# Performance work log

Hardware: AMD Instinct MI355X
Metric: run time of the kernel (lower is better)

## Reference

```python
import jax, jax.numpy as jnp
import numpy as np

DN = ('NCDHW', 'DHWIO', 'NCDHW')
EPS = 1e-5


def conv_s2(x, W):
    # ME kernel-3 stride-2 conv: out[o] = sum_{d in {-1,0,1}^3} W[d] @ in[2o+d]
    return jax.lax.conv_general_dilated(x, W, (2, 2, 2), ((1, 1),) * 3,
                                        dimension_numbers=DN)


def deconv_s2(x, W):
    # ME kernel-3 stride-2 transpose conv: out[2i+d] += W[d] @ in[i]
    # == zero-stuffed (lhs_dilation=2) conv with spatially flipped kernel.
    Wf = W[::-1, ::-1, ::-1]
    return jax.lax.conv_general_dilated(x, Wf, (1, 1, 1), ((1, 2),) * 3,
                                        lhs_dilation=(2, 2, 2),
                                        dimension_numbers=DN)


def pool2(m):
    # output coordinate existence for stride-2: any occupied voxel in 2x2x2 block
    return jax.lax.reduce_window(m, 0.0, jax.lax.max,
                                 (1, 1, 2, 2, 2), (1, 1, 2, 2, 2), 'VALID')


def bn_relu(x, m, gamma, beta):
    # MinkowskiBatchNorm: stats over occupied points only (mask m in {0,1})
    cnt = m.sum()
    mean = (x * m).sum(axis=(0, 2, 3, 4)) / cnt            # [C]
    xc = (x - mean[None, :, None, None, None]) * m
    var = (xc * xc).sum(axis=(0, 2, 3, 4)) / cnt           # biased var, [C]
    scale = (gamma / jnp.sqrt(var + EPS))[None, :, None, None, None]
    y = xc * scale + beta[None, :, None, None, None] * m
    return jax.nn.relu(y) * m


def occ_head(x, m, w, b):
    # 1x1 conv (C->1, bias) + sigmoid at occupied sites
    logit = jnp.einsum('bcdhw,c->bdhw', x, w)[:, None] + b
    return jax.nn.sigmoid(logit) * m


def setup_inputs() -> dict:
    key = jax.random.key(0)
    ks = jax.random.split(key, 24)
    B, Cin, Cout, G = 2, 3, 3, 96
    feats = jax.random.normal(ks[0], (B, Cin, G, G, G), jnp.float32)
    mask = jax.random.bernoulli(ks[1], 0.2, (B, 1, G, G, G))

    def w(k, ci, co):
        return jax.random.normal(k, (3, 3, 3, ci, co), jnp.float32) * np.float32((2.0 / (27 * co)) ** 0.5)

    enc = [16, 32, 64, 128]
    d = {'feats': feats, 'mask': mask}
    d['W1'] = w(ks[2], Cin, 16); d['g1'] = jnp.ones(16); d['b1'] = jnp.zeros(16)
    d['W2'] = w(ks[3], 16, 32);  d['g2'] = jnp.ones(32); d['b2'] = jnp.zeros(32)
    d['W3'] = w(ks[4], 32, 64);  d['g3'] = jnp.ones(64); d['b3'] = jnp.zeros(64)
    d['W4'] = w(ks[5], 64, 128); d['g4'] = jnp.ones(128); d['b4'] = jnp.zeros(128)
    d['Wt4'] = w(ks[6], 128, 64); d['gd4'] = jnp.ones(64); d['bd4'] = jnp.zeros(64)
    d['wo4'] = jax.random.normal(ks[7], (64,), jnp.float32) * 0.1; d['bo4'] = jnp.zeros((1,))
    d['Wt3'] = w(ks[8], 64, 32); d['gd3'] = jnp.ones(32); d['bd3'] = jnp.zeros(32)
    d['wo3'] = jax.random.normal(ks[9], (32,), jnp.float32) * 0.1; d['bo3'] = jnp.zeros((1,))
    d['Wt2'] = w(ks[10], 32, 16); d['gd2'] = jnp.ones(16); d['bd2'] = jnp.zeros(16)
    d['wo2'] = jax.random.normal(ks[11], (16,), jnp.float32) * 0.1; d['bo2'] = jnp.zeros((1,))
    d['Wt1'] = w(ks[12], 16, Cout)
    d['wo1'] = jax.random.normal(ks[13], (Cout,), jnp.float32) * 0.1; d['bo1'] = jnp.zeros((1,))
    return d


def reference(feats, mask, W1, g1, b1, W2, g2, b2, W3, g3, b3, W4, g4, b4,
              Wt4, gd4, bd4, wo4, bo4, Wt3, gd3, bd3, wo3, bo3,
              Wt2, gd2, bd2, wo2, bo2, Wt1, wo1, bo1):
    m0 = mask.astype(feats.dtype)
    m1 = pool2(m0); m2 = pool2(m1); m3 = pool2(m2); m4 = pool2(m3)
    x = feats * m0
    e0 = bn_relu(conv_s2(x, W1), m1, g1, b1)    # [B,16,48^3]
    e1 = bn_relu(conv_s2(e0, W2), m2, g2, b2)   # [B,32,24^3]
    e2 = bn_relu(conv_s2(e1, W3), m3, g3, b3)   # [B,64,12^3]
    e3 = bn_relu(conv_s2(e2, W4), m4, g4, b4)   # [B,128,6^3]
    d3 = bn_relu(deconv_s2(e3, Wt4), m3, gd4, bd4)
    p4 = occ_head(d3, m3, wo4, bo4)
    d3 = d3 + e2
    d2 = bn_relu(deconv_s2(d3, Wt3), m2, gd3, bd3)
    p3 = occ_head(d2, m2, wo3, bo3)
    d2 = d2 + e1
    d1 = bn_relu(deconv_s2(d2, Wt2), m1, gd2, bd2)
    p2 = occ_head(d1, m1, wo2, bo2)
    d1 = d1 + e0
    d0 = jax.nn.sigmoid(deconv_s2(d1, Wt1)) * m0  # Decoder1: transpose conv + sigmoid
    p1 = occ_head(d0, m0, wo1, bo1)
    return (d0, p4, p3, p2, p1)
```

## Files before the change

kernel.cpp:

```cpp
#include <hip/hip_runtime.h>
#include <math.h>

#define CDIV(a,b) (((a)+(b)-1)/(b))
typedef unsigned int u32;

__device__ __forceinline__ float sigmoidf_(float x) { return 1.f / (1.f + __expf(-x)); }

__global__ void k_detect(const u32* __restrict__ w, int n, u32* __restrict__ flag) {
    u32 local = 0;
    for (int i = blockIdx.x * blockDim.x + threadIdx.x; i < n; i += gridDim.x * blockDim.x) {
        u32 v = w[i];
        if (v == 0x3F800000u) local |= 2u;
        else if (v > 1u)      local |= 1u;
    }
    if (local) atomicOr(flag, local);
}

__global__ void k_expand(const void* __restrict__ mraw, const u32* __restrict__ flag,
                         float* __restrict__ m, int n) {
    int i = blockIdx.x * blockDim.x + threadIdx.x;
    if (i >= n) return;
    u32 f = *flag;
    float v;
    if (f & 2u)      v = ((const float*)mraw)[i];
    else if (f & 1u) v = ((const unsigned char*)mraw)[i] ? 1.f : 0.f;
    else             v = ((const int*)mraw)[i] ? 1.f : 0.f;
    m[i] = v;
}

__global__ void k_pool(const float* __restrict__ mi, float* __restrict__ mo,
                       float* __restrict__ cnt, int Si, int n) {
    int So = Si >> 1;
    int i = blockIdx.x * blockDim.x + threadIdx.x;
    float v = 0.f;
    if (i < n) {
        int x = i % So; int t = i / So;
        int y = t % So; t /= So;
        int z = t % So; int b = t / So;
        const float* p = mi + (size_t)b * Si * Si * Si;
        #pragma unroll
        for (int dz = 0; dz < 2; dz++)
        #pragma unroll
        for (int dy = 0; dy < 2; dy++)
        #pragma unroll
        for (int dx = 0; dx < 2; dx++) {
            float q = p[((size_t)(2 * z + dz) * Si + (2 * y + dy)) * Si + (2 * x + dx)];
            v = fmaxf(v, q);
        }
        mo[i] = v;
    }
    __shared__ float red[256];
    red[threadIdx.x] = v; __syncthreads();
    for (int s = 128; s > 0; s >>= 1) {
        if (threadIdx.x < s) red[threadIdx.x] += red[threadIdx.x + s];
        __syncthreads();
    }
    if (threadIdx.x == 0) atomicAdd(cnt, red[0]);
}

__global__ __launch_bounds__(256)
void k_conv1(const float* __restrict__ feats, const float* __restrict__ m0,
             const float* __restrict__ W, float* __restrict__ out,
             const float* __restrict__ m1, float* __restrict__ stats) {
    constexpr int SIN = 96;
    constexpr int V0 = SIN * SIN * SIN, V1 = 48 * 48 * 48;
    __shared__ __align__(16) float wlds[27 * 3 * 16];
    __shared__ float sred[4][32];
    for (int idx = threadIdx.x; idx < 27 * 3 * 16; idx += 256) wlds[idx] = W[idx];
    __syncthreads();
    int chunk = blockIdx.x * 256 + threadIdx.x;
    int b = chunk / V1; int s = chunk - b * V1;
    int x = s % 48, y = (s / 48) % 48, z = s / 2304;
    float acc[16];
    #pragma unroll
    for (int co = 0; co < 16; ++co) acc[co] = 0.f;
    const float* bi = feats + (size_t)b * 3 * V0;
    const float* bm = m0 + (size_t)b * V0;
    #pragma unroll
    for (int kz = 0; kz < 3; ++kz) {
        int iz = 2 * z - 1 + kz; if (iz < 0) continue;
        #pragma unroll
        for (int ky = 0; ky < 3; ++ky) {
            int iy = 2 * y - 1 + ky; if (iy < 0) continue;
            #pragma unroll
            for (int kx = 0; kx < 3; ++kx) {
                int ix = 2 * x - 1 + kx; if (ix < 0) continue;
                int off = (iz * SIN + iy) * SIN + ix;
                float mv = bm[off];
                if (mv != 0.f) {
                    float f0 = bi[off], f1 = bi[V0 + off], f2 = bi[2 * V0 + off];
                    const float* wp = &wlds[((kz * 3 + ky) * 3 + kx) * 48];
                    #pragma unroll
                    for (int co = 0; co < 16; ++co)
                        acc[co] += f0 * wp[co] + f1 * wp[16 + co] + f2 * wp[32 + co];
                }
            }
        }
    }
    float mm = m1[chunk];
    #pragma unroll
    for (int co = 0; co < 16; ++co) acc[co] *= mm;
    float* op = out + (size_t)chunk * 16;
    #pragma unroll
    for (int q = 0; q < 4; ++q)
        *reinterpret_cast<float4*>(op + q * 4) =
            make_float4(acc[q*4], acc[q*4+1], acc[q*4+2], acc[q*4+3]);
    float s1[16], s2[16];
    #pragma unroll
    for (int co = 0; co < 16; ++co) { s1[co] = acc[co]; s2[co] = acc[co] * acc[co]; }
    #pragma unroll
    for (int co = 0; co < 16; ++co)
        for (int off = 1; off < 64; off <<= 1) {
            s1[co] += __shfl_xor(s1[co], off);
            s2[co] += __shfl_xor(s2[co], off);
        }
    int lane = threadIdx.x & 63, wid = threadIdx.x >> 6;
    if (lane == 0) {
        #pragma unroll
        for (int co = 0; co < 16; ++co) { sred[wid][co] = s1[co]; sred[wid][16 + co] = s2[co]; }
    }
    __syncthreads();
    if (threadIdx.x < 32) {
        int t = threadIdx.x;
        float v = sred[0][t] + sred[1][t] + sred[2][t] + sred[3][t];
        int addr = (t < 16) ? t : (128 + t - 16);
        atomicAdd(&stats[addr], v);
    }
}

template<int CI, int CO, int CO_T, int SIN, int SOUT, bool STATS>
__global__ __launch_bounds__(256)
void k_convCL(const float* __restrict__ in, const float* __restrict__ W,
              float* __restrict__ out, const float* __restrict__ mout,
              float* __restrict__ stats) {
    constexpr int SIN3 = SIN * SIN * SIN, SOUT3 = SOUT * SOUT * SOUT;
    constexpr int NW = 27 * CI * CO_T;
    __shared__ __align__(16) float wlds[NW];
    __shared__ float sred[STATS ? 4 : 1][2 * CO_T];
    const int cobase = blockIdx.y * CO_T;
    for (int idx = threadIdx.x; idx < NW; idx += 256) {
        int t = idx / (CI * CO_T);
        int rem = idx - t * CI * CO_T;
        int ci = rem / CO_T, co = rem - ci * CO_T;
        wlds[idx] = W[(size_t)(t * CI + ci) * CO + cobase + co];
    }
    __syncthreads();
    int chunk = blockIdx.x * 256 + threadIdx.x;
    bool active = chunk < 2 * SOUT3;
    if (!STATS && !active) return;
    float acc[CO_T];
    #pragma unroll
    for (int co = 0; co < CO_T; ++co) acc[co] = 0.f;
    if (active) {
        int b = chunk / SOUT3, s = chunk - b * SOUT3;
        int x = s % SOUT, y = (s / SOUT) % SOUT, z = s / (SOUT * SOUT);
        const float* bi = in + (size_t)b * SIN3 * CI;
        #pragma unroll
        for (int kz = 0; kz < 3; ++kz) {
            int iz = 2 * z - 1 + kz; if (iz < 0 || iz >= SIN) continue;
            #pragma unroll
            for (int ky = 0; ky < 3; ++ky) {
                int iy = 2 * y - 1 + ky; if (iy < 0 || iy >= SIN) continue;
                #pragma unroll
                for (int kx = 0; kx < 3; ++kx) {
                    int ix = 2 * x - 1 + kx; if (ix < 0 || ix >= SIN) continue;
                    const float* p = bi + (size_t)((iz * SIN + iy) * SIN + ix) * CI;
                    const float* wp = &wlds[((kz * 3 + ky) * 3 + kx) * CI * CO_T];
                    #pragma unroll
                    for (int cq = 0; cq < CI / 4; ++cq) {
                        float4 v = *reinterpret_cast<const float4*>(p + cq * 4);
                        const float* wq = wp + cq * 4 * CO_T;
                        float vv[4] = {v.x, v.y, v.z, v.w};
                        #pragma unroll
                        for (int jj = 0; jj < 4; ++jj)
                        #pragma unroll
                        for (int co = 0; co < CO_T; ++co)
                            acc[co] += vv[jj] * wq[jj * CO_T + co];
                    }
                }
            }
        }
        float mm = mout[chunk];
        #pragma unroll
        for (int co = 0; co < CO_T; ++co) acc[co] *= mm;
        float* op = out + (size_t)chunk * CO + cobase;
        #pragma unroll
        for (int q = 0; q < CO_T / 4; ++q)
            *reinterpret_cast<float4*>(op + q * 4) =
                make_float4(acc[q*4], acc[q*4+1], acc[q*4+2], acc[q*4+3]);
    }
    if constexpr (STATS) {
        float s1[CO_T], s2[CO_T];
        #pragma unroll
        for (int co = 0; co < CO_T; ++co) { s1[co] = acc[co]; s2[co] = acc[co] * acc[co]; }
        #pragma unroll
        for (int co = 0; co < CO_T; ++co)
            for (int off = 1; off < 64; off <<= 1) {
                s1[co] += __shfl_xor(s1[co], off);
                s2[co] += __shfl_xor(s2[co], off);
            }
        int lane = threadIdx.x & 63, wid = threadIdx.x >> 6;
        if (lane == 0) {
            #pragma unroll
            for (int co = 0; co < CO_T; ++co) { sred[wid][co] = s1[co]; sred[wid][CO_T + co] = s2[co]; }
        }
        __syncthreads();
        if (threadIdx.x < 2 * CO_T) {
            int t = threadIdx.x;
            float v = sred[0][t] + sred[1][t] + sred[2][t] + sred[3][t];
            int addr = (t < CO_T) ? (cobase + t) : (128 + cobase + t - CO_T);
            atomicAdd(&stats[addr], v);
        }
    }
}

template<int CI, int CO, int CO_T, int SIN, bool STATS>
__global__ __launch_bounds__(256)
void k_deconvG(const float* __restrict__ in, const float* __restrict__ W,
               const float* __restrict__ mout, float* __restrict__ out,
               float* __restrict__ stats) {
    constexpr int SOUT = 2 * SIN;
    constexpr int SIN3 = SIN * SIN * SIN, SOUT3 = SOUT * SOUT * SOUT;
    constexpr int NW = 27 * CI * CO_T;
    __shared__ __align__(16) float wlds[NW];
    __shared__ float sred[STATS ? 4 : 1][2 * CO_T];
    const int cobase = blockIdx.y * CO_T;
    for (int idx = threadIdx.x; idx < NW; idx += 256) {
        int w = idx / (CI * CO_T);
        int rem = idx - w * (CI * CO_T);
        int ci = rem / CO_T, co = rem - ci * CO_T;
        wlds[idx] = W[(size_t)(w * CI + ci) * CO + cobase + co];
    }
    __syncthreads();
    int chunk = blockIdx.x * 256 + threadIdx.x;
    bool active = chunk < 2 * SOUT3;
    if (!STATS && !active) return;
    float acc[CO_T];
    #pragma unroll
    for (int co = 0; co < CO_T; ++co) acc[co] = 0.f;
    if (active) {
        int b = chunk / SOUT3, s = chunk - b * SOUT3;
        int x = s % SOUT, y = (s / SOUT) % SOUT, z = s / (SOUT * SOUT);
        int z0 = z >> 1, y0 = y >> 1, x0 = x >> 1;
        int nz = ((z & 1) && (z0 + 1 < SIN)) ? 2 : 1;
        int ny = ((y & 1) && (y0 + 1 < SIN)) ? 2 : 1;
        int nx = ((x & 1) && (x0 + 1 < SIN)) ? 2 : 1;
        int wz0 = (z & 1) ? 2 : 1, wy0 = (y & 1) ? 2 : 1, wx0 = (x & 1) ? 2 : 1;
        const float* bi = in + (size_t)b * SIN3 * CI;
        #pragma unroll 1
        for (int tz = 0; tz < nz; ++tz) {
            int iz = z0 + tz, wz = tz ? 0 : wz0;
            #pragma unroll 1
            for (int ty = 0; ty < ny; ++ty) {
                int iy = y0 + ty, wy = ty ? 0 : wy0;
                #pragma unroll 1
                for (int tx = 0; tx < nx; ++tx) {
                    int ix = x0 + tx, wx = tx ? 0 : wx0;
                    const float* p = bi + (size_t)((iz * SIN + iy) * SIN + ix) * CI;
                    const float* wb = &wlds[((wz * 3 + wy) * 3 + wx) * CI * CO_T];
                    #pragma unroll 8
                    for (int cq = 0; cq < CI / 4; ++cq) {
                        float4 v = *reinterpret_cast<const float4*>(p + cq * 4);
                        const float* wq = wb + cq * 4 * CO_T;
                        float vv[4] = {v.x, v.y, v.z, v.w};
                        #pragma unroll
                        for (int jj = 0; jj < 4; ++jj)
                        #pragma unroll
                        for (int co = 0; co < CO_T; ++co)
                            acc[co] += vv[jj] * wq[jj * CO_T + co];
                    }
                }
            }
        }
        float mm = mout[chunk];
        #pragma unroll
        for (int co = 0; co < CO_T; ++co) acc[co] *= mm;
        float* op = out + (size_t)chunk * CO + cobase;
        #pragma unroll
        for (int q = 0; q < CO_T / 4; ++q)
            *reinterpret_cast<float4*>(op + q * 4) =
                make_float4(acc[q*4], acc[q*4+1], acc[q*4+2], acc[q*4+3]);
    }
    if constexpr (STATS) {
        float s1[CO_T], s2[CO_T];
        #pragma unroll
        for (int co = 0; co < CO_T; ++co) { s1[co] = acc[co]; s2[co] = acc[co] * acc[co]; }
        #pragma unroll
        for (int co = 0; co < CO_T; ++co)
            for (int off = 1; off < 64; off <<= 1) {
                s1[co] += __shfl_xor(s1[co], off);
                s2[co] += __shfl_xor(s2[co], off);
            }
        int lane = threadIdx.x & 63, wid = threadIdx.x >> 6;
        if (lane == 0) {
            #pragma unroll
            for (int co = 0; co < CO_T; ++co) { sred[wid][co] = s1[co]; sred[wid][CO_T + co] = s2[co]; }
        }
        __syncthreads();
        if (threadIdx.x < 2 * CO_T) {
            int t = threadIdx.x;
            float v = sred[0][t] + sred[1][t] + sred[2][t] + sred[3][t];
            int addr = (t < CO_T) ? (cobase + t) : (128 + cobase + t - CO_T);
            atomicAdd(&stats[addr], v);
        }
    }
}

__global__ __launch_bounds__(256)
void k_deconv_final(const float* __restrict__ in, const float* __restrict__ W,
                    const float* __restrict__ m0, float* __restrict__ out,
                    const float* __restrict__ ow, const float* __restrict__ ob,
                    float* __restrict__ p1out) {
    constexpr int SI = 48, SO = 96;
    constexpr int SI3 = SI * SI * SI, SO3 = SO * SO * SO;
    __shared__ __align__(16) float wlds[27 * 16 * 4];
    for (int idx = threadIdx.x; idx < 27 * 16 * 4; idx += 256) {
        int w = idx >> 6; int rem = idx & 63;
        int ci = rem >> 2, co = rem & 3;
        wlds[idx] = (co < 3) ? W[(size_t)(w * 16 + ci) * 3 + co] : 0.f;
    }
    __syncthreads();
    int t = blockIdx.x * 256 + threadIdx.x;
    int b = t / (SO3 / 4); int s = t - b * (SO3 / 4);
    int x4 = s % 24; int y = (s / 24) % SO; int z = s / (24 * SO);
    int x0 = x4 * 4, kxb = x4 * 2;
    int izs[2], wzs[2], nz = 1;
    if (z & 1) { izs[0] = z >> 1; wzs[0] = 2; int i2 = (z >> 1) + 1;
                 if (i2 < SI) { izs[1] = i2; wzs[1] = 0; nz = 2; } }
    else       { izs[0] = z >> 1; wzs[0] = 1; }
    int iys[2], wys[2], ny = 1;
    if (y & 1) { iys[0] = y >> 1; wys[0] = 2; int i2 = (y >> 1) + 1;
                 if (i2 < SI) { iys[1] = i2; wys[1] = 0; ny = 2; } }
    else       { iys[0] = y >> 1; wys[0] = 1; }
    bool has2 = (kxb + 2 < SI);
    float acc[4][3];
    #pragma unroll
    for (int o = 0; o < 4; ++o)
    #pragma unroll
    for (int c = 0; c < 3; ++c) acc[o][c] = 0.f;
    const float* bi = in + (size_t)b * SI3 * 16;
    #pragma unroll 1
    for (int tz = 0; tz < nz; ++tz)
    #pragma unroll 1
    for (int ty = 0; ty < ny; ++ty) {
        const float* vp = bi + ((size_t)(izs[tz] * SI + iys[ty]) * SI + kxb) * 16;
        float v[3][16];
        #pragma unroll
        for (int q = 0; q < 4; ++q) {
            float4 a = *reinterpret_cast<const float4*>(vp + q * 4);
            float4 bq = *reinterpret_cast<const float4*>(vp + 16 + q * 4);
            v[0][q*4] = a.x; v[0][q*4+1] = a.y; v[0][q*4+2] = a.z; v[0][q*4+3] = a.w;
            v[1][q*4] = bq.x; v[1][q*4+1] = bq.y; v[1][q*4+2] = bq.z; v[1][q*4+3] = bq.w;
            float4 cq = has2 ? *reinterpret_cast<const float4*>(vp + 32 + q * 4)
                             : make_float4(0.f, 0.f, 0.f, 0.f);
            v[2][q*4] = cq.x; v[2][q*4+1] = cq.y; v[2][q*4+2] = cq.z; v[2][q*4+3] = cq.w;
        }
        const float* wb = &wlds[(wzs[tz] * 3 + wys[ty]) * 3 * 64];
        #pragma unroll
        for (int ci = 0; ci < 16; ++ci) {
            float4 w0 = *reinterpret_cast<const float4*>(wb + ci * 4);
            float4 w1 = *reinterpret_cast<const float4*>(wb + 64 + ci * 4);
            float4 w2 = *reinterpret_cast<const float4*>(wb + 128 + ci * 4);
            float v0 = v[0][ci], v1 = v[1][ci], v2 = v[2][ci];
            acc[0][0] += v0 * w1.x; acc[0][1] += v0 * w1.y; acc[0][2] += v0 * w1.z;
            acc[1][0] += v0 * w2.x + v1 * w0.x;
            acc[1][1] += v0 * w2.y + v1 * w0.y;
            acc[1][2] += v0 * w2.z + v1 * w0.z;
            acc[2][0] += v1 * w1.x; acc[2][1] += v1 * w1.y; acc[2][2] += v1 * w1.z;
            acc[3][0] += v1 * w2.x + v2 * w0.x;
            acc[3][1] += v1 * w2.y + v2 * w0.y;
            acc[3][2] += v1 * w2.z + v2 * w0.z;
        }
    }
    int row = (z * SO + y) * SO + x0;
    float4 mm = *reinterpret_cast<const float4*>(m0 + (size_t)b * SO3 + row);
    float mv[4] = {mm.x, mm.y, mm.z, mm.w};
    const float w0o = ow[0], w1o = ow[1], w2o = ow[2], bo = ob[0];
    float yv[3][4], p1[4];
    #pragma unroll
    for (int o = 0; o < 4; ++o) {
        float y0 = sigmoidf_(acc[o][0]) * mv[o];
        float y1 = sigmoidf_(acc[o][1]) * mv[o];
        float y2 = sigmoidf_(acc[o][2]) * mv[o];
        yv[0][o] = y0; yv[1][o] = y1; yv[2][o] = y2;
        p1[o] = sigmoidf_(y0 * w0o + y1 * w1o + y2 * w2o + bo) * mv[o];
    }
    float* ob0 = out + (size_t)b * 3 * SO3 + row;
    #pragma unroll
    for (int c = 0; c < 3; ++c)
        *reinterpret_cast<float4*>(ob0 + (size_t)c * SO3) =
            make_float4(yv[c][0], yv[c][1], yv[c][2], yv[c][3]);
    *reinterpret_cast<float4*>(p1out + (size_t)b * SO3 + row) =
        make_float4(p1[0], p1[1], p1[2], p1[3]);
}

template<int C, bool OCC, bool ADD>
__global__ __launch_bounds__(256)
void k_bnCL(float* __restrict__ x, const float* __restrict__ m,
            const float* __restrict__ stats, const float* __restrict__ cnt,
            const float* __restrict__ g, const float* __restrict__ be,
            const float* __restrict__ skip, const float* __restrict__ ow,
            const float* __restrict__ ob, float* __restrict__ oo, int totq) {
    constexpr int CQ = C / 4;
    int i = blockIdx.x * 256 + threadIdx.x;
    if (i >= totq) return;
    int vox = i / CQ, cq = i - vox * CQ;
    int c0 = 4 * cq;
    float cn = *cnt;
    float4 s1 = *reinterpret_cast<const float4*>(stats + c0);
    float4 s2 = *reinterpret_cast<const float4*>(stats + 128 + c0);
    float sc[4], sh[4];
    {
        float mean0 = s1.x / cn, mean1 = s1.y / cn, mean2 = s1.z / cn, mean3 = s1.w / cn;
        float v0 = s2.x / cn - mean0 * mean0, v1 = s2.y / cn - mean1 * mean1;
        float v2 = s2.z / cn - mean2 * mean2, v3 = s2.w / cn - mean3 * mean3;
        sc[0] = g[c0] * rsqrtf(v0 + 1e-5f);   sh[0] = be[c0] - mean0 * sc[0];
        sc[1] = g[c0+1] * rsqrtf(v1 + 1e-5f); sh[1] = be[c0+1] - mean1 * sc[1];
        sc[2] = g[c0+2] * rsqrtf(v2 + 1e-5f); sh[2] = be[c0+2] - mean2 * sc[2];
        sc[3] = g[c0+3] * rsqrtf(v3 + 1e-5f); sh[3] = be[c0+3] - mean3 * sc[3];
    }
    float mm = m[vox];
    float4 xv = *reinterpret_cast<const float4*>(x + (size_t)i * 4);
    float y[4];
    y[0] = fmaxf(xv.x * sc[0] + sh[0], 0.f) * mm;
    y[1] = fmaxf(xv.y * sc[1] + sh[1], 0.f) * mm;
    y[2] = fmaxf(xv.z * sc[2] + sh[2], 0.f) * mm;
    y[3] = fmaxf(xv.w * sc[3] + sh[3], 0.f) * mm;
    if constexpr (OCC) {
        float po = y[0] * ow[c0] + y[1] * ow[c0+1] + y[2] * ow[c0+2] + y[3] * ow[c0+3];
        #pragma unroll
        for (int off = 1; off < CQ; off <<= 1) po += __shfl_xor(po, off);
        if (cq == 0) oo[vox] = sigmoidf_(po + ob[0]) * mm;
    }
    if constexpr (ADD) {
        float4 sk = *reinterpret_cast<const float4*>(skip + (size_t)i * 4);
        y[0] += sk.x; y[1] += sk.y; y[2] += sk.z; y[3] += sk.w;
    }
    *reinterpret_cast<float4*>(x + (size_t)i * 4) = make_float4(y[0], y[1], y[2], y[3]);
}

extern "C" void kernel_launch(void* const* d_in, const int* in_sizes, int n_in,
                              void* d_out, int out_size, void* d_ws, size_t ws_size,
                              hipStream_t stream) {
    (void)in_sizes; (void)n_in; (void)out_size; (void)ws_size;
    const float* feats = (const float*)d_in[0];
    const void*  mraw  = d_in[1];
    const float* W1 = (const float*)d_in[2];
    const float* g1 = (const float*)d_in[3];  const float* b1 = (const float*)d_in[4];
    const float* W2 = (const float*)d_in[5];
    const float* g2 = (const float*)d_in[6];  const float* b2 = (const float*)d_in[7];
    const float* W3 = (const float*)d_in[8];
    const float* g3 = (const float*)d_in[9];  const float* b3 = (const float*)d_in[10];
    const float* W4 = (const float*)d_in[11];
    const float* g4 = (const float*)d_in[12]; const float* b4 = (const float*)d_in[13];
    const float* Wt4 = (const float*)d_in[14];
    const float* gd4 = (const float*)d_in[15]; const float* bd4 = (const float*)d_in[16];
    const float* wo4 = (const float*)d_in[17]; const float* bo4 = (const float*)d_in[18];
    const float* Wt3 = (const float*)d_in[19];
    const float* gd3 = (const float*)d_in[20]; const float* bd3 = (const float*)d_in[21];
    const float* wo3 = (const float*)d_in[22]; const float* bo3 = (const float*)d_in[23];
    const float* Wt2 = (const float*)d_in[24];
    const float* gd2 = (const float*)d_in[25]; const float* bd2 = (const float*)d_in[26];
    const float* wo2 = (const float*)d_in[27]; const float* bo2 = (const float*)d_in[28];
    const float* Wt1 = (const float*)d_in[29];
    const float* wo1 = (const float*)d_in[30]; const float* bo1 = (const float*)d_in[31];

    float* out = (float*)d_out;

    const int NB = 2;
    const int V0 = 96 * 96 * 96;
    const int V1 = 48 * 48 * 48;
    const int V2 = 24 * 24 * 24;
    const int V3 = 12 * 12 * 12;
    const int V4 = 6 * 6 * 6;

    const size_t OFF_P4 = (size_t)NB * 3 * V0;
    const size_t OFF_P3 = OFF_P4 + (size_t)NB * V3;
    const size_t OFF_P2 = OFF_P3 + (size_t)NB * V2;
    const size_t OFF_P1 = OFF_P2 + (size_t)NB * V1;

    float* ws = (float*)d_ws;
    size_t o = 0;
    auto alloc = [&](size_t n) { float* p = ws + o; o += ((n + 63) / 64) * 64; return p; };
    u32*   flag  = (u32*)alloc(64);
    float* cnt   = alloc(64);
    float* stats = alloc(8 * 512);
    float* m0f   = alloc((size_t)NB * V0);
    float* m1f   = alloc((size_t)NB * V1);
    float* m2f   = alloc((size_t)NB * V2);
    float* m3f   = alloc((size_t)NB * V3);
    float* m4f   = alloc((size_t)NB * V4);
    float* e0    = alloc((size_t)NB * V1 * 16);
    float* e1    = alloc((size_t)NB * V2 * 32);
    float* e2    = alloc((size_t)NB * V3 * 64);
    float* e3    = alloc((size_t)NB * V4 * 128);
    float* d3    = alloc((size_t)NB * V3 * 64);
    float* d2    = alloc((size_t)NB * V2 * 32);
    float* d1    = alloc((size_t)NB * V1 * 16);
    (void)alloc(1024);

    const int T = 256;

    hipMemsetAsync(flag, 0, (64 + 64 + 8 * 512) * sizeof(float), stream);

    k_detect<<<256, T, 0, stream>>>((const u32*)mraw, (NB * V0) / 4, flag);
    k_expand<<<CDIV(NB * V0, T), T, 0, stream>>>(mraw, flag, m0f, NB * V0);
    k_pool<<<CDIV(NB * V1, T), T, 0, stream>>>(m0f, m1f, &cnt[0], 96, NB * V1);
    k_pool<<<CDIV(NB * V2, T), T, 0, stream>>>(m1f, m2f, &cnt[1], 48, NB * V2);
    k_pool<<<CDIV(NB * V3, T), T, 0, stream>>>(m2f, m3f, &cnt[2], 24, NB * V3);
    k_pool<<<CDIV(NB * V4, T), T, 0, stream>>>(m3f, m4f, &cnt[3], 12, NB * V4);

    k_conv1<<<864, T, 0, stream>>>(feats, m0f, W1, e0, m1f, stats + 0 * 512);
    k_bnCL<16, false, false><<<3456, T, 0, stream>>>(
        e0, m1f, stats + 0 * 512, &cnt[0], g1, b1, nullptr, nullptr, nullptr, nullptr, NB * V1 * 4);

    k_convCL<16, 32, 8, 48, 24, true><<<dim3(108, 4), T, 0, stream>>>(
        e0, W2, e1, m2f, stats + 1 * 512);
    k_bnCL<32, false, false><<<864, T, 0, stream>>>(
        e1, m2f, stats + 1 * 512, &cnt[1], g2, b2, nullptr, nullptr, nullptr, nullptr, NB * V2 * 8);

    k_convCL<32, 64, 4, 24, 12, true><<<dim3(14, 16), T, 0, stream>>>(
        e1, W3, e2, m3f, stats + 2 * 512);
    k_bnCL<64, false, false><<<216, T, 0, stream>>>(
        e2, m3f, stats + 2 * 512, &cnt[2], g3, b3, nullptr, nullptr, nullptr, nullptr, NB * V3 * 16);

    k_convCL<64, 128, 4, 12, 6, true><<<dim3(2, 32), T, 0, stream>>>(
        e2, W4, e3, m4f, stats + 3 * 512);
    k_bnCL<128, false, false><<<54, T, 0, stream>>>(
        e3, m4f, stats + 3 * 512, &cnt[3], g4, b4, nullptr, nullptr, nullptr, nullptr, NB * V4 * 32);

    k_deconvG<128, 64, 4, 6, true><<<dim3(14, 16), T, 0, stream>>>(
        e3, Wt4, m3f, d3, stats + 4 * 512);
    k_bnCL<64, true, true><<<216, T, 0, stream>>>(
        d3, m3f, stats + 4 * 512, &cnt[2], gd4, bd4, e2, wo4, bo4, out + OFF_P4, NB * V3 * 16);

    k_deconvG<64, 32, 8, 12, true><<<dim3(108, 4), T, 0, stream>>>(
        d3, Wt3, m2f, d2, stats + 5 * 512);
    k_bnCL<32, true, true><<<864, T, 0, stream>>>(
        d2, m2f, stats + 5 * 512, &cnt[1], gd3, bd3, e1, wo3, bo3, out + OFF_P3, NB * V2 * 8);

    k_deconvG<32, 16, 16, 24, true><<<dim3(864, 1), T, 0, stream>>>(
        d2, Wt2, m1f, d1, stats + 6 * 512);
    k_bnCL<16, true, true><<<3456, T, 0, stream>>>(
        d1, m1f, stats + 6 * 512, &cnt[0], gd2, bd2, e0, wo2, bo2, out + OFF_P2, NB * V1 * 4);

    k_deconv_final<<<1728, T, 0, stream>>>(d1, Wt1, m0f, out, wo1, bo1, out + OFF_P1);
}
```

Before: 415.8 us.

## Register-block multiple x outputs per thread in stride-2 conv and deconv kernels

Result: slower. 638.6 us (+53.6%).

```diff
diff --git a/kernel.cpp b/kernel.cpp
--- a/kernel.cpp
+++ b/kernel.cpp
@@ -125,6 +125,259 @@
         float v = sred[0][t] + sred[1][t] + sred[2][t] + sred[3][t];
         int addr = (t < 16) ? t : (128 + t - 16);
         atomicAdd(&stats[addr], v);
+    }
+}
+
+template<int CI, int CO, int CO_T, int SP_T, int SIN, int SOUT, bool STATS>
+__global__ __launch_bounds__(256)
+void k_convS(const float* __restrict__ in, const float* __restrict__ W,
+             float* __restrict__ out, const float* __restrict__ mout,
+             float* __restrict__ stats) {
+    constexpr int SIN3 = SIN * SIN * SIN, SOUT3 = SOUT * SOUT * SOUT;
+    constexpr int XG = SOUT / SP_T;
+    constexpr int NTH = 2 * SOUT * SOUT * XG;
+    constexpr int WST = CI * CO_T + 4;
+    __shared__ __align__(16) float wlds[27 * WST];
+    __shared__ float sred[4][2 * CO_T];
+    const int cobase = blockIdx.y * CO_T;
+    for (int idx = threadIdx.x; idx < 27 * CI * CO_T; idx += 256) {
+        int t = idx / (CI * CO_T);
+        int rem = idx - t * (CI * CO_T);
+        int ci = rem / CO_T, co = rem - ci * CO_T;
+        wlds[t * WST + ci * CO_T + co] = W[(size_t)(t * CI + ci) * CO + cobase + co];
+    }
+    __syncthreads();
+    int chunk = blockIdx.x * 256 + threadIdx.x;
+    bool active = chunk < NTH;
+    float acc[SP_T][CO_T];
+    #pragma unroll
+    for (int j = 0; j < SP_T; ++j)
+    #pragma unroll
+    for (int co = 0; co < CO_T; ++co) acc[j][co] = 0.f;
+    if (active) {
+        int xg = chunk % XG; int q = chunk / XG;
+        int y = q % SOUT; q /= SOUT;
+        int z = q % SOUT; int b = q / SOUT;
+        int x0 = SP_T * xg;
+        int xbi = 2 * x0 - 1;
+        const float* bi = in + (size_t)b * SIN3 * CI;
+        #pragma unroll
+        for (int kz = 0; kz < 3; ++kz) {
+            int iz = 2 * z - 1 + kz; if (iz < 0) continue;
+            #pragma unroll
+            for (int ky = 0; ky < 3; ++ky) {
+                int iy = 2 * y - 1 + ky; if (iy < 0) continue;
+                const float* rp = bi + (size_t)((iz * SIN + iy) * SIN) * CI;
+                #pragma unroll
+                for (int cq = 0; cq < CI / 4; ++cq) {
+                    float v[2 * SP_T + 1][4];
+                    #pragma unroll
+                    for (int t = 0; t < 2 * SP_T + 1; ++t) {
+                        int ix = xbi + t;
+                        float4 q4 = make_float4(0.f, 0.f, 0.f, 0.f);
+                        if (ix >= 0)
+                            q4 = *reinterpret_cast<const float4*>(rp + (size_t)ix * CI + cq * 4);
+                        v[t][0] = q4.x; v[t][1] = q4.y; v[t][2] = q4.z; v[t][3] = q4.w;
+                    }
+                    #pragma unroll
+                    for (int kx = 0; kx < 3; ++kx) {
+                        const float* wb = &wlds[((kz * 3 + ky) * 3 + kx) * WST + cq * 4 * CO_T];
+                        #pragma unroll
+                        for (int jj = 0; jj < 4; ++jj) {
+                            float wv[CO_T];
+                            #pragma unroll
+                            for (int co = 0; co < CO_T; ++co) wv[co] = wb[jj * CO_T + co];
+                            #pragma unroll
+                            for (int j = 0; j < SP_T; ++j) {
+                                float iv = v[2 * j + kx][jj];
+                                #pragma unroll
+                                for (int co = 0; co < CO_T; ++co) acc[j][co] += iv * wv[co];
+                            }
+                        }
+                    }
+                }
+            }
+        }
+        int vbase = b * SOUT3 + (z * SOUT + y) * SOUT + x0;
+        #pragma unroll
+        for (int j = 0; j < SP_T; ++j) {
+            float mm = mout[vbase + j];
+            #pragma unroll
+            for (int co = 0; co < CO_T; ++co) acc[j][co] *= mm;
+            float* op = out + (size_t)(vbase + j) * CO + cobase;
+            #pragma unroll
+            for (int q4 = 0; q4 < CO_T / 4; ++q4)
+                *reinterpret_cast<float4*>(op + q4 * 4) =
+                    make_float4(acc[j][q4*4], acc[j][q4*4+1], acc[j][q4*4+2], acc[j][q4*4+3]);
+        }
+    }
+    if constexpr (STATS) {
+        float s1[CO_T], s2[CO_T];
+        #pragma unroll
+        for (int co = 0; co < CO_T; ++co) {
+            float a = 0.f, b2 = 0.f;
+            #pragma unroll
+            for (int j = 0; j < SP_T; ++j) { a += acc[j][co]; b2 += acc[j][co] * acc[j][co]; }
+            s1[co] = a; s2[co] = b2;
+        }
+        #pragma unroll
+        for (int co = 0; co < CO_T; ++co)
+            for (int off = 1; off < 64; off <<= 1) {
+                s1[co] += __shfl_xor(s1[co], off);
+                s2[co] += __shfl_xor(s2[co], off);
+            }
+        int lane = threadIdx.x & 63, wid = threadIdx.x >> 6;
+        if (lane == 0) {
+            #pragma unroll
+            for (int co = 0; co < CO_T; ++co) { sred[wid][co] = s1[co]; sred[wid][CO_T + co] = s2[co]; }
+        }
+        __syncthreads();
+        if (threadIdx.x < 2 * CO_T) {
+            int t = threadIdx.x;
+            float v = sred[0][t] + sred[1][t] + sred[2][t] + sred[3][t];
+            int addr = (t < CO_T) ? (cobase + t) : (128 + cobase + t - CO_T);
+            atomicAdd(&stats[addr], v);
+        }
+    }
+}
+
+template<int CI, int CO, int CO_T, int SP_T, int SIN, bool STATS>
+__global__ __launch_bounds__(256)
+void k_deconvP(const float* __restrict__ in, const float* __restrict__ W,
+               const float* __restrict__ mout, float* __restrict__ out,
+               float* __restrict__ stats) {
+    constexpr int SOUT = 2 * SIN;
+    constexpr int SIN3 = SIN * SIN * SIN, SOUT3 = SOUT * SOUT * SOUT;
+    constexpr int GX = SOUT / (2 * SP_T);
+    constexpr int NTH = 2 * SOUT * SOUT * 2 * GX;
+    constexpr int HALF = NTH / 2;
+    constexpr int WST = CI * CO_T + 4;
+    __shared__ __align__(16) float wlds[27 * WST];
+    __shared__ float sred[4][2 * CO_T];
+    const int cobase = blockIdx.y * CO_T;
+    for (int idx = threadIdx.x; idx < 27 * CI * CO_T; idx += 256) {
+        int w = idx / (CI * CO_T);
+        int rem = idx - w * (CI * CO_T);
+        int ci = rem / CO_T, co = rem - ci * CO_T;
+        wlds[w * WST + ci * CO_T + co] = W[(size_t)(w * CI + ci) * CO + cobase + co];
+    }
+    __syncthreads();
+    int chunk = blockIdx.x * 256 + threadIdx.x;
+    bool active = chunk < NTH;
+    float acc[SP_T][CO_T];
+    #pragma unroll
+    for (int j = 0; j < SP_T; ++j)
+    #pragma unroll
+    for (int co = 0; co < CO_T; ++co) acc[j][co] = 0.f;
+    if (active) {
+        int p = (chunk >= HALF) ? 1 : 0;
+        int r = chunk - p * HALF;
+        int g = r % GX; int q = r / GX;
+        int y = q % SOUT; q /= SOUT;
+        int z = q % SOUT; int b = q / SOUT;
+        int xb = SP_T * g;
+        int z0 = z >> 1, y0 = y >> 1;
+        int nz = ((z & 1) && (z0 + 1 < SIN)) ? 2 : 1;
+        int ny = ((y & 1) && (y0 + 1 < SIN)) ? 2 : 1;
+        int wz0 = (z & 1) ? 2 : 1, wy0 = (y & 1) ? 2 : 1;
+        bool lastok = (xb + SP_T < SIN);
+        const float* bi = in + (size_t)b * SIN3 * CI;
+        #pragma unroll 1
+        for (int tz = 0; tz < nz; ++tz) {
+            int iz = z0 + tz, wz = tz ? 0 : wz0;
+            #pragma unroll 1
+            for (int ty = 0; ty < ny; ++ty) {
+                int iy = y0 + ty, wy = ty ? 0 : wy0;
+                const float* rp = bi + (size_t)((iz * SIN + iy) * SIN + xb) * CI;
+                #pragma unroll
+                for (int cq = 0; cq < CI / 4; ++cq) {
+                    float v[SP_T + 1][4];
+                    #pragma unroll
+                    for (int t = 0; t < SP_T; ++t) {
+                        float4 q4 = *reinterpret_cast<const float4*>(rp + (size_t)t * CI + cq * 4);
+                        v[t][0] = q4.x; v[t][1] = q4.y; v[t][2] = q4.z; v[t][3] = q4.w;
+                    }
+                    if (p) {
+                        float4 q4 = make_float4(0.f, 0.f, 0.f, 0.f);
+                        if (lastok)
+                            q4 = *reinterpret_cast<const float4*>(rp + (size_t)SP_T * CI + cq * 4);
+                        v[SP_T][0] = q4.x; v[SP_T][1] = q4.y; v[SP_T][2] = q4.z; v[SP_T][3] = q4.w;
+                    }
+                    if (p == 0) {
+                        const float* wb = &wlds[((wz * 3 + wy) * 3 + 1) * WST + cq * 4 * CO_T];
+                        #pragma unroll
+                        for (int jj = 0; jj < 4; ++jj) {
+                            float wv[CO_T];
+                            #pragma unroll
+                            for (int co = 0; co < CO_T; ++co) wv[co] = wb[jj * CO_T + co];
+                            #pragma unroll
+                            for (int j = 0; j < SP_T; ++j) {
+                                float iv = v[j][jj];
+                                #pragma unroll
+                                for (int co = 0; co < CO_T; ++co) acc[j][co] += iv * wv[co];
+                            }
+                        }
+                    } else {
+                        const float* wb2 = &wlds[((wz * 3 + wy) * 3 + 2) * WST + cq * 4 * CO_T];
+                        const float* wb0 = &wlds[((wz * 3 + wy) * 3 + 0) * WST + cq * 4 * CO_T];
+                        #pragma unroll
+                        for (int jj = 0; jj < 4; ++jj) {
+                            float wv2[CO_T], wv0[CO_T];
+                            #pragma unroll
+                            for (int co = 0; co < CO_T; ++co) { wv2[co] = wb2[jj * CO_T + co]; wv0[co] = wb0[jj * CO_T + co]; }
+                            #pragma unroll
+                            for (int j = 0; j < SP_T; ++j) {
+                                float ivA = v[j][jj], ivB = v[j + 1][jj];
+                                #pragma unroll
+                                for (int co = 0; co < CO_T; ++co)
+                                    acc[j][co] += ivA * wv2[co] + ivB * wv0[co];
+                            }
+                        }
+                    }
+                }
+            }
+        }
+        int sp = b * SOUT3 + (z * SOUT + y) * SOUT;
+        #pragma unroll
+        for (int j = 0; j < SP_T; ++j) {
+            int vox = sp + 2 * (xb + j) + p;
+            float mm = mout[vox];
+            #pragma unroll
+            for (int co = 0; co < CO_T; ++co) acc[j][co] *= mm;
+            float* op = out + (size_t)vox * CO + cobase;
+            #pragma unroll
+            for (int q4 = 0; q4 < CO_T / 4; ++q4)
+                *reinterpret_cast<float4*>(op + q4 * 4) =
+                    make_float4(acc[j][q4*4], acc[j][q4*4+1], acc[j][q4*4+2], acc[j][q4*4+3]);
+        }
+    }
+    if constexpr (STATS) {
+        float s1[CO_T], s2[CO_T];
+        #pragma unroll
+        for (int co = 0; co < CO_T; ++co) {
+            float a = 0.f, b2 = 0.f;
+            #pragma unroll
+            for (int j = 0; j < SP_T; ++j) { a += acc[j][co]; b2 += acc[j][co] * acc[j][co]; }
+            s1[co] = a; s2[co] = b2;
+        }
+        #pragma unroll
+        for (int co = 0; co < CO_T; ++co)
+            for (int off = 1; off < 64; off <<= 1) {
+                s1[co] += __shfl_xor(s1[co], off);
+                s2[co] += __shfl_xor(s2[co], off);
+            }
+        int lane = threadIdx.x & 63, wid = threadIdx.x >> 6;
+        if (lane == 0) {
+            #pragma unroll
+            for (int co = 0; co < CO_T; ++co) { sred[wid][co] = s1[co]; sred[wid][CO_T + co] = s2[co]; }
+        }
+        __syncthreads();
+        if (threadIdx.x < 2 * CO_T) {
+            int t = threadIdx.x;
+            float v = sred[0][t] + sred[1][t] + sred[2][t] + sred[3][t];
+            int addr = (t < CO_T) ? (cobase + t) : (128 + cobase + t - CO_T);
+            atomicAdd(&stats[addr], v);
+        }
     }
 }
 
@@ -170,98 +423,6 @@
                     for (int cq = 0; cq < CI / 4; ++cq) {
                         float4 v = *reinterpret_cast<const float4*>(p + cq * 4);
                         const float* wq = wp + cq * 4 * CO_T;
-                        float vv[4] = {v.x, v.y, v.z, v.w};
-                        #pragma unroll
-                        for (int jj = 0; jj < 4; ++jj)
-                        #pragma unroll
-                        for (int co = 0; co < CO_T; ++co)
-                            acc[co] += vv[jj] * wq[jj * CO_T + co];
-                    }
-                }
-            }
-        }
-        float mm = mout[chunk];
-        #pragma unroll
-        for (int co = 0; co < CO_T; ++co) acc[co] *= mm;
-        float* op = out + (size_t)chunk * CO + cobase;
-        #pragma unroll
-        for (int q = 0; q < CO_T / 4; ++q)
-            *reinterpret_cast<float4*>(op + q * 4) =
-                make_float4(acc[q*4], acc[q*4+1], acc[q*4+2], acc[q*4+3]);
-    }
-    if constexpr (STATS) {
-        float s1[CO_T], s2[CO_T];
-        #pragma unroll
-        for (int co = 0; co < CO_T; ++co) { s1[co] = acc[co]; s2[co] = acc[co] * acc[co]; }
-        #pragma unroll
-        for (int co = 0; co < CO_T; ++co)
-            for (int off = 1; off < 64; off <<= 1) {
-                s1[co] += __shfl_xor(s1[co], off);
-                s2[co] += __shfl_xor(s2[co], off);
-            }
-        int lane = threadIdx.x & 63, wid = threadIdx.x >> 6;
-        if (lane == 0) {
-            #pragma unroll
-            for (int co = 0; co < CO_T; ++co) { sred[wid][co] = s1[co]; sred[wid][CO_T + co] = s2[co]; }
-        }
-        __syncthreads();
-        if (threadIdx.x < 2 * CO_T) {
-            int t = threadIdx.x;
-            float v = sred[0][t] + sred[1][t] + sred[2][t] + sred[3][t];
-            int addr = (t < CO_T) ? (cobase + t) : (128 + cobase + t - CO_T);
-            atomicAdd(&stats[addr], v);
-        }
-    }
-}
-
-template<int CI, int CO, int CO_T, int SIN, bool STATS>
-__global__ __launch_bounds__(256)
-void k_deconvG(const float* __restrict__ in, const float* __restrict__ W,
-               const float* __restrict__ mout, float* __restrict__ out,
-               float* __restrict__ stats) {
-    constexpr int SOUT = 2 * SIN;
-    constexpr int SIN3 = SIN * SIN * SIN, SOUT3 = SOUT * SOUT * SOUT;
-    constexpr int NW = 27 * CI * CO_T;
-    __shared__ __align__(16) float wlds[NW];
-    __shared__ float sred[STATS ? 4 : 1][2 * CO_T];
-    const int cobase = blockIdx.y * CO_T;
-    for (int idx = threadIdx.x; idx < NW; idx += 256) {
-        int w = idx / (CI * CO_T);
-        int rem = idx - w * (CI * CO_T);
-        int ci = rem / CO_T, co = rem - ci * CO_T;
-        wlds[idx] = W[(size_t)(w * CI + ci) * CO + cobase + co];
-    }
-    __syncthreads();
-    int chunk = blockIdx.x * 256 + threadIdx.x;
-    bool active = chunk < 2 * SOUT3;
-    if (!STATS && !active) return;
-    float acc[CO_T];
-    #pragma unroll
-    for (int co = 0; co < CO_T; ++co) acc[co] = 0.f;
-    if (active) {
-        int b = chunk / SOUT3, s = chunk - b * SOUT3;
-        int x = s % SOUT, y = (s / SOUT) % SOUT, z = s / (SOUT * SOUT);
-        int z0 = z >> 1, y0 = y >> 1, x0 = x >> 1;
-        int nz = ((z & 1) && (z0 + 1 < SIN)) ? 2 : 1;
-        int ny = ((y & 1) && (y0 + 1 < SIN)) ? 2 : 1;
-        int nx = ((x & 1) && (x0 + 1 < SIN)) ? 2 : 1;
-        int wz0 = (z & 1) ? 2 : 1, wy0 = (y & 1) ? 2 : 1, wx0 = (x & 1) ? 2 : 1;
-        const float* bi = in + (size_t)b * SIN3 * CI;
-        #pragma unroll 1
-        for (int tz = 0; tz < nz; ++tz) {
-            int iz = z0 + tz, wz = tz ? 0 : wz0;
-            #pragma unroll 1
-            for (int ty = 0; ty < ny; ++ty) {
-                int iy = y0 + ty, wy = ty ? 0 : wy0;
-                #pragma unroll 1
-                for (int tx = 0; tx < nx; ++tx) {
-                    int ix = x0 + tx, wx = tx ? 0 : wx0;
-                    const float* p = bi + (size_t)((iz * SIN + iy) * SIN + ix) * CI;
-                    const float* wb = &wlds[((wz * 3 + wy) * 3 + wx) * CI * CO_T];
-                    #pragma unroll 8
-                    for (int cq = 0; cq < CI / 4; ++cq) {
-                        float4 v = *reinterpret_cast<const float4*>(p + cq * 4);
-                        const float* wq = wb + cq * 4 * CO_T;
                         float vv[4] = {v.x, v.y, v.z, v.w};
                         #pragma unroll
                         for (int jj = 0; jj < 4; ++jj)
@@ -514,12 +675,12 @@
     k_bnCL<16, false, false><<<3456, T, 0, stream>>>(
         e0, m1f, stats + 0 * 512, &cnt[0], g1, b1, nullptr, nullptr, nullptr, nullptr, NB * V1 * 4);
 
-    k_convCL<16, 32, 8, 48, 24, true><<<dim3(108, 4), T, 0, stream>>>(
+    k_convS<16, 32, 8, 2, 48, 24, true><<<dim3(54, 4), T, 0, stream>>>(
         e0, W2, e1, m2f, stats + 1 * 512);
     k_bnCL<32, false, false><<<864, T, 0, stream>>>(
         e1, m2f, stats + 1 * 512, &cnt[1], g2, b2, nullptr, nullptr, nullptr, nullptr, NB * V2 * 8);
 
-    k_convCL<32, 64, 4, 24, 12, true><<<dim3(14, 16), T, 0, stream>>>(
+    k_convS<32, 64, 4, 2, 24, 12, true><<<dim3(7, 16), T, 0, stream>>>(
         e1, W3, e2, m3f, stats + 2 * 512);
     k_bnCL<64, false, false><<<216, T, 0, stream>>>(
         e2, m3f, stats + 2 * 512, &cnt[2], g3, b3, nullptr, nullptr, nullptr, nullptr, NB * V3 * 16);
@@ -529,17 +690,17 @@
     k_bnCL<128, false, false><<<54, T, 0, stream>>>(
         e3, m4f, stats + 3 * 512, &cnt[3], g4, b4, nullptr, nullptr, nullptr, nullptr, NB * V4 * 32);
 
-    k_deconvG<128, 64, 4, 6, true><<<dim3(14, 16), T, 0, stream>>>(
+    k_deconvP<128, 64, 4, 2, 6, true><<<dim3(7, 16), T, 0, stream>>>(
         e3, Wt4, m3f, d3, stats + 4 * 512);
     k_bnCL<64, true, true><<<216, T, 0, stream>>>(
         d3, m3f, stats + 4 * 512, &cnt[2], gd4, bd4, e2, wo4, bo4, out + OFF_P4, NB * V3 * 16);
 
-    k_deconvG<64, 32, 8, 12, true><<<dim3(108, 4), T, 0, stream>>>(
+    k_deconvP<64, 32, 8, 4, 12, true><<<dim3(27, 4), T, 0, stream>>>(
         d3, Wt3, m2f, d2, stats + 5 * 512);
     k_bnCL<32, true, true><<<864, T, 0, stream>>>(
         d2, m2f, stats + 5 * 512, &cnt[1], gd3, bd3, e1, wo3, bo3, out + OFF_P3, NB * V2 * 8);
 
-    k_deconvG<32, 16, 16, 24, true><<<dim3(864, 1), T, 0, stream>>>(
+    k_deconvP<32, 16, 16, 4, 24, true><<<dim3(216, 1), T, 0, stream>>>(
         d2, Wt2, m1f, d1, stats + 6 * 512);
     k_bnCL<16, true, true><<<3456, T, 0, stream>>>(
         d1, m1f, stats + 6 * 512, &cnt[0], gd2, bd2, e0, wo2, bo2, out + OFF_P2, NB * V1 * 4);
```

## Register-tile deconvolution over x-parity with multiple outputs per thread

Applied to the files above, without the earlier changes.

Result: slower. 452.6 us (+8.8%).

```diff
diff --git a/kernel.cpp b/kernel.cpp
--- a/kernel.cpp
+++ b/kernel.cpp
@@ -214,38 +214,47 @@
     }
 }
 
-template<int CI, int CO, int CO_T, int SIN, bool STATS>
+template<int CI, int CO, int CO_T, int SP_T, int SIN, bool STATS>
 __global__ __launch_bounds__(256)
-void k_deconvG(const float* __restrict__ in, const float* __restrict__ W,
+void k_deconvA(const float* __restrict__ in, const float* __restrict__ W,
                const float* __restrict__ mout, float* __restrict__ out,
                float* __restrict__ stats) {
     constexpr int SOUT = 2 * SIN;
     constexpr int SIN3 = SIN * SIN * SIN, SOUT3 = SOUT * SOUT * SOUT;
-    constexpr int NW = 27 * CI * CO_T;
-    __shared__ __align__(16) float wlds[NW];
+    constexpr int GX = SIN / SP_T;
+    constexpr int HALF = 2 * SOUT * SOUT * GX;
+    constexpr int NTH = 2 * HALF;
+    constexpr int WST = CI * CO_T + 4;
+    __shared__ __align__(16) float wlds[27 * WST];
     __shared__ float sred[STATS ? 4 : 1][2 * CO_T];
     const int cobase = blockIdx.y * CO_T;
-    for (int idx = threadIdx.x; idx < NW; idx += 256) {
+    for (int idx = threadIdx.x; idx < 27 * CI * CO_T; idx += 256) {
         int w = idx / (CI * CO_T);
         int rem = idx - w * (CI * CO_T);
         int ci = rem / CO_T, co = rem - ci * CO_T;
-        wlds[idx] = W[(size_t)(w * CI + ci) * CO + cobase + co];
+        wlds[w * WST + ci * CO_T + co] = W[(size_t)(w * CI + ci) * CO + cobase + co];
     }
     __syncthreads();
     int chunk = blockIdx.x * 256 + threadIdx.x;
-    bool active = chunk < 2 * SOUT3;
-    if (!STATS && !active) return;
-    float acc[CO_T];
-    #pragma unroll
-    for (int co = 0; co < CO_T; ++co) acc[co] = 0.f;
+    bool active = chunk < NTH;
+    float acc[SP_T][CO_T];
+    #pragma unroll
+    for (int j = 0; j < SP_T; ++j)
+    #pragma unroll
+    for (int co = 0; co < CO_T; ++co) acc[j][co] = 0.f;
+    int p = 0, g = 0, y = 0, z = 0, b = 0;
     if (active) {
-        int b = chunk / SOUT3, s = chunk - b * SOUT3;
-        int x = s % SOUT, y = (s / SOUT) % SOUT, z = s / (SOUT * SOUT);
-        int z0 = z >> 1, y0 = y >> 1, x0 = x >> 1;
+        p = (chunk >= HALF) ? 1 : 0;
+        int r = chunk - p * HALF;
+        g = r % GX; int q = r / GX;
+        y = q % SOUT; q /= SOUT;
+        z = q % SOUT; b = q / SOUT;
+        int x0 = SP_T * g;
+        int z0 = z >> 1, y0 = y >> 1;
         int nz = ((z & 1) && (z0 + 1 < SIN)) ? 2 : 1;
         int ny = ((y & 1) && (y0 + 1 < SIN)) ? 2 : 1;
-        int nx = ((x & 1) && (x0 + 1 < SIN)) ? 2 : 1;
-        int wz0 = (z & 1) ? 2 : 1, wy0 = (y & 1) ? 2 : 1, wx0 = (x & 1) ? 2 : 1;
+        int wz0 = (z & 1) ? 2 : 1, wy0 = (y & 1) ? 2 : 1;
+        bool lastok = (x0 + SP_T < SIN);
         const float* bi = in + (size_t)b * SIN3 * CI;
         #pragma unroll 1
         for (int tz = 0; tz < nz; ++tz) {
@@ -253,38 +262,82 @@
             #pragma unroll 1
             for (int ty = 0; ty < ny; ++ty) {
                 int iy = y0 + ty, wy = ty ? 0 : wy0;
-                #pragma unroll 1
-                for (int tx = 0; tx < nx; ++tx) {
-                    int ix = x0 + tx, wx = tx ? 0 : wx0;
-                    const float* p = bi + (size_t)((iz * SIN + iy) * SIN + ix) * CI;
-                    const float* wb = &wlds[((wz * 3 + wy) * 3 + wx) * CI * CO_T];
-                    #pragma unroll 8
-                    for (int cq = 0; cq < CI / 4; ++cq) {
-                        float4 v = *reinterpret_cast<const float4*>(p + cq * 4);
-                        const float* wq = wb + cq * 4 * CO_T;
-                        float vv[4] = {v.x, v.y, v.z, v.w};
+                const float* rp = bi + (size_t)((iz * SIN + iy) * SIN + x0) * CI;
+                #pragma unroll 2
+                for (int cq = 0; cq < CI / 4; ++cq) {
+                    float v[SP_T + 1][4];
+                    #pragma unroll
+                    for (int t = 0; t < SP_T; ++t) {
+                        float4 q4 = *reinterpret_cast<const float4*>(rp + (size_t)t * CI + cq * 4);
+                        v[t][0] = q4.x; v[t][1] = q4.y; v[t][2] = q4.z; v[t][3] = q4.w;
+                    }
+                    if (p) {
+                        float4 q4 = make_float4(0.f, 0.f, 0.f, 0.f);
+                        if (lastok)
+                            q4 = *reinterpret_cast<const float4*>(rp + (size_t)SP_T * CI + cq * 4);
+                        v[SP_T][0] = q4.x; v[SP_T][1] = q4.y; v[SP_T][2] = q4.z; v[SP_T][3] = q4.w;
+                    }
+                    if (p == 0) {
+                        const float* wb = &wlds[((wz * 3 + wy) * 3 + 1) * WST + cq * 4 * CO_T];
                         #pragma unroll
-                        for (int jj = 0; jj < 4; ++jj)
+                        for (int jj = 0; jj < 4; ++jj) {
+                            float wv[CO_T];
+                            #pragma unroll
+                            for (int co = 0; co < CO_T; ++co) wv[co] = wb[jj * CO_T + co];
+                            #pragma unroll
+                            for (int j = 0; j < SP_T; ++j) {
+                                float iv = v[j][jj];
+                                #pragma unroll
+                                for (int co = 0; co < CO_T; ++co) acc[j][co] += iv * wv[co];
+                            }
+                        }
+                    } else {
+                        const float* wb2 = &wlds[((wz * 3 + wy) * 3 + 2) * WST + cq * 4 * CO_T];
+                        const float* wb0 = &wlds[((wz * 3 + wy) * 3 + 0) * WST + cq * 4 * CO_T];
                         #pragma unroll
-                        for (int co = 0; co < CO_T; ++co)
-                            acc[co] += vv[jj] * wq[jj * CO_T + co];
+                        for (int jj = 0; jj < 4; ++jj) {
+                            float wv2[CO_T], wv0[CO_T];
+                            #pragma unroll
+                            for (int co = 0; co < CO_T; ++co) {
+                                wv2[co] = wb2[jj * CO_T + co];
+                                wv0[co] = wb0[jj * CO_T + co];
+                            }
+                            #pragma unroll
+                            for (int j = 0; j < SP_T; ++j) {
+                                float ivA = v[j][jj], ivB = v[j + 1][jj];
+                                #pragma unroll
+                                for (int co = 0; co < CO_T; ++co)
+                                    acc[j][co] += ivA * wv2[co] + ivB * wv0[co];
+                            }
+                        }
                     }
                 }
             }
         }
-        float mm = mout[chunk];
-        #pragma unroll
-        for (int co = 0; co < CO_T; ++co) acc[co] *= mm;
-        float* op = out + (size_t)chunk * CO + cobase;
-        #pragma unroll
-        for (int q = 0; q < CO_T / 4; ++q)
-            *reinterpret_cast<float4*>(op + q * 4) =
-                make_float4(acc[q*4], acc[q*4+1], acc[q*4+2], acc[q*4+3]);
+        int sp = b * SOUT3 + (z * SOUT + y) * SOUT;
+        int x0o = 2 * SP_T * g + p;
+        #pragma unroll
+        for (int j = 0; j < SP_T; ++j) {
+            int vox = sp + x0o + 2 * j;
+            float mm = mout[vox];
+            #pragma unroll
+            for (int co = 0; co < CO_T; ++co) acc[j][co] *= mm;
+            float* op = out + (size_t)vox * CO + cobase;
+            #pragma unroll
+            for (int q4 = 0; q4 < CO_T / 4; ++q4)
+                *reinterpret_cast<float4*>(op + q4 * 4) =
+                    make_float4(acc[j][q4*4], acc[j][q4*4+1], acc[j][q4*4+2], acc[j][q4*4+3]);
+        }
     }
     if constexpr (STATS) {
         float s1[CO_T], s2[CO_T];
         #pragma unroll
-        for (int co = 0; co < CO_T; ++co) { s1[co] = acc[co]; s2[co] = acc[co] * acc[co]; }
+        for (int co = 0; co < CO_T; ++co) {
+            float a = 0.f, b2 = 0.f;
+            #pragma unroll
+            for (int j = 0; j < SP_T; ++j) { a += acc[j][co]; b2 += acc[j][co] * acc[j][co]; }
+            s1[co] = a; s2[co] = b2;
+        }
         #pragma unroll
         for (int co = 0; co < CO_T; ++co)
             for (int off = 1; off < 64; off <<= 1) {
@@ -529,17 +582,17 @@
     k_bnCL<128, false, false><<<54, T, 0, stream>>>(
         e3, m4f, stats + 3 * 512, &cnt[3], g4, b4, nullptr, nullptr, nullptr, nullptr, NB * V4 * 32);
 
-    k_deconvG<128, 64, 4, 6, true><<<dim3(14, 16), T, 0, stream>>>(
+    k_deconvA<128, 64, 4, 2, 6, true><<<dim3(7, 16), T, 0, stream>>>(
         e3, Wt4, m3f, d3, stats + 4 * 512);
     k_bnCL<64, true, true><<<216, T, 0, stream>>>(
         d3, m3f, stats + 4 * 512, &cnt[2], gd4, bd4, e2, wo4, bo4, out + OFF_P4, NB * V3 * 16);
 
-    k_deconvG<64, 32, 8, 12, true><<<dim3(108, 4), T, 0, stream>>>(
+    k_deconvA<64, 32, 8, 2, 12, true><<<dim3(54, 4), T, 0, stream>>>(
         d3, Wt3, m2f, d2, stats + 5 * 512);
     k_bnCL<32, true, true><<<864, T, 0, stream>>>(
         d2, m2f, stats + 5 * 512, &cnt[1], gd3, bd3, e1, wo3, bo3, out + OFF_P3, NB * V2 * 8);
 
-    k_deconvG<32, 16, 16, 24, true><<<dim3(864, 1), T, 0, stream>>>(
+    k_deconvA<32, 16, 16, 4, 24, true><<<dim3(216, 1), T, 0, stream>>>(
         d2, Wt2, m1f, d1, stats + 6 * 512);
     k_bnCL<16, true, true><<<3456, T, 0, stream>>>(
         d1, m1f, stats + 6 * 512, &cnt[0], gd2, bd2, e0, wo2, bo2, out + OFF_P2, NB * V1 * 4);
```
